# Performance work log

Measured on AMD Instinct MI355X. Metric: run time of the kernel, lower is better.

## Reference

```python
import jax, jax.numpy as jnp
import numpy as np

NA, NB, C = 50000, 50000, 128
E = 800000
S, IN, H, NBASES = 8, 64, 64, 8
NUM_LAYERS = 2
EPS = 1e-5


def setup_inputs() -> dict:
    key = jax.random.key(0)
    ks = jax.random.split(key, 16)
    inp = {
        'x_a': jax.random.normal(ks[0], (NA, C), jnp.float32),
        'x_b': jax.random.normal(ks[1], (NB, C), jnp.float32),
        'schema_x': jax.random.normal(ks[2], (S, IN), jnp.float32),
        'edge_ab': jax.random.randint(ks[3], (2, E), 0, NA, jnp.int32),
        'edge_ba': jax.random.randint(ks[4], (2, E), 0, NA, jnp.int32),
        'edge_aa': jax.random.randint(ks[5], (2, E), 0, NA, jnp.int32),
        'schema_edge_index': jax.random.randint(ks[6], (2, 24), 0, S, jnp.int32),
        'pre_W': jax.random.normal(ks[7], (H, IN), jnp.float32) * (1.0 / np.sqrt(IN)),
        'pre_b': jnp.zeros((H,), jnp.float32),
        'gcn_W': jax.random.normal(ks[8], (H, H), jnp.float32) * (1.0 / np.sqrt(H)),
        'gcn_b': jnp.zeros((H,), jnp.float32),
        'coeff_W': jax.random.normal(ks[9], (NBASES, 2 * H), jnp.float32) * (1.0 / np.sqrt(2 * H)),
        'coeff_b': jnp.zeros((NBASES,), jnp.float32),
        'bases': jax.random.normal(ks[10], (NUM_LAYERS, NBASES, C, C), jnp.float32) * (1.0 / np.sqrt(C)),
        'sage_bias': jnp.zeros((NUM_LAYERS, 3, C), jnp.float32),
        'ln_w': jnp.ones((NUM_LAYERS, 2, C), jnp.float32),
        'ln_b': jnp.zeros((NUM_LAYERS, 2, C), jnp.float32),
    }
    return inp


def _gcn_conv(x, ei, W, b):
    # PyG GCNConv: add self-loops, symmetric normalization, then linear.
    n = x.shape[0]
    loop = jnp.arange(n, dtype=ei.dtype)
    src = jnp.concatenate([ei[0], loop])
    dst = jnp.concatenate([ei[1], loop])
    deg = jax.ops.segment_sum(jnp.ones_like(dst, jnp.float32), dst, num_segments=n)
    dinv = jax.lax.rsqrt(jnp.maximum(deg, 1e-12))
    norm = dinv[src] * dinv[dst]  # [E+n]
    xw = x @ W.T  # [n, H]
    out = jax.ops.segment_sum(xw[src] * norm[:, None], dst, num_segments=n)
    return out + b


def _sage_conv(x_src, x_dst, ei, W, b):
    # PyG SAGEConv, aggr='mean': lin_l(mean_j x_src[j]) + lin_r(x_dst); lin_l.weight == lin_r.weight == W.
    n_dst = x_dst.shape[0]
    msg_sum = jax.ops.segment_sum(x_src[ei[0]], ei[1], num_segments=n_dst)
    cnt = jax.ops.segment_sum(jnp.ones(ei.shape[1], x_src.dtype), ei[1], num_segments=n_dst)
    mean = msg_sum / jnp.maximum(cnt, 1.0)[:, None]
    return (mean + x_dst) @ W.T + b


def _layer_norm(x, w, b):
    mu = jnp.mean(x, axis=-1, keepdims=True)
    var = jnp.mean(jnp.square(x - mu), axis=-1, keepdims=True)
    return (x - mu) * jax.lax.rsqrt(var + EPS) * w + b


def _edge_weight(sf_src, sf_dst, coeff_W, coeff_b, bases_l):
    combined = jnp.concatenate([sf_src, sf_dst], axis=0)  # [2H]
    coeffs = combined @ coeff_W.T + coeff_b  # [NBASES]
    return jnp.einsum('i,ijk->jk', coeffs, bases_l)  # [C, C]


def reference(x_a, x_b, schema_x, edge_ab, edge_ba, edge_aa, schema_edge_index,
              pre_W, pre_b, gcn_W, gcn_b, coeff_W, coeff_b, bases,
              sage_bias, ln_w, ln_b):
    # Schema GCN over the tiny table-level graph. table_to_index: a->0, b->1.
    h = schema_x @ pre_W.T + pre_b
    ori = h
    sf = jax.nn.relu(_gcn_conv(h, schema_edge_index, gcn_W, gcn_b))  # [S, H]

    for l in range(NUM_LAYERS):
        bases_l = bases[l]
        W_ab = _edge_weight(sf[0], sf[1], coeff_W, coeff_b, bases_l)
        W_ba = _edge_weight(sf[1], sf[0], coeff_W, coeff_b, bases_l)
        W_aa = _edge_weight(sf[0], sf[0], coeff_W, coeff_b, bases_l)
        # HeteroConv(aggr='sum'): sum SAGE outputs per destination node type.
        out_b = _sage_conv(x_a, x_b, edge_ab, W_ab, sage_bias[l, 0])
        out_a = (_sage_conv(x_b, x_a, edge_ba, W_ba, sage_bias[l, 1])
                 + _sage_conv(x_a, x_a, edge_aa, W_aa, sage_bias[l, 2]))
        x_a = jax.nn.relu(_layer_norm(out_a, ln_w[l, 0], ln_b[l, 0]))
        x_b = jax.nn.relu(_layer_norm(out_b, ln_w[l, 1], ln_b[l, 1]))

    return x_a, x_b, sf, ori
```

## Files before the change

kernel.cpp:

```cpp
#include <hip/hip_runtime.h>

#define NA 50000
#define NB 50000
#define NN 50000
#define CDIM 128
#define EDGES 800000
#define SS 8
#define INDIM 64
#define HDIM 64
#define NBASES 8
#define NBUCK 98
#define BSH 9

typedef __attribute__((ext_vector_type(8))) short bf16x8;
typedef __attribute__((ext_vector_type(4))) float f32x4;


__device__ __forceinline__ unsigned short f2bf(float f) {
    unsigned u = __float_as_uint(f);
    return (unsigned short)((u + 0x7FFFu + ((u >> 16) & 1u)) >> 16);
}

__global__ __launch_bounds__(512) void schema_kernel(
    const float* __restrict__ schema_x, const int* __restrict__ sei,
    const float* __restrict__ preW, const float* __restrict__ preb,
    const float* __restrict__ gcnW, const float* __restrict__ gcnb,
    const float* __restrict__ coW, const float* __restrict__ cob,
    float* __restrict__ out_sf, float* __restrict__ out_ori,
    float* __restrict__ coeffs)
{
    __shared__ float h[SS][HDIM];
    __shared__ float xw[SS][HDIM];
    __shared__ float sf[SS][HDIM];
    __shared__ float deg[SS];
    __shared__ float nrm[32];
    __shared__ int es[32], ed[32];

    int t = threadIdx.x;
    int i = t >> 6, j = t & 63;

    float acc = preb[j];
    for (int k = 0; k < INDIM; k++) acc += schema_x[i * INDIM + k] * preW[j * INDIM + k];
    h[i][j] = acc;
    out_ori[i * HDIM + j] = acc;
    if (t < SS) deg[t] = 0.0f;
    __syncthreads();

    if (t < 32) {
        int s, d;
        if (t < 24) { s = sei[t]; d = sei[24 + t]; }
        else        { s = t - 24; d = t - 24; }
        es[t] = s; ed[t] = d;
        atomicAdd(&deg[d], 1.0f);
    }
    __syncthreads();
    if (t < 32) {
        nrm[t] = rsqrtf(fmaxf(deg[es[t]], 1e-12f)) * rsqrtf(fmaxf(deg[ed[t]], 1e-12f));
    }
    float a2 = 0.0f;
    for (int k = 0; k < HDIM; k++) a2 += h[i][k] * gcnW[j * HDIM + k];
    xw[i][j] = a2;
    __syncthreads();

    float o = gcnb[j];
    for (int e = 0; e < 32; e++) {
        if (ed[e] == i) o += xw[es[e]][j] * nrm[e];
    }
    float s = fmaxf(o, 0.0f);
    sf[i][j] = s;
    out_sf[i * HDIM + j] = s;
    __syncthreads();

    if (t < 24) {
        int ty = t >> 3, ii = t & 7;
        int srow = (ty == 1) ? 1 : 0;
        int drow = (ty == 0) ? 1 : 0;
        float a = cob[ii];
        for (int k = 0; k < HDIM; k++) a += sf[srow][k] * coW[ii * (2 * HDIM) + k];
        for (int k = 0; k < HDIM; k++) a += sf[drow][k] * coW[ii * (2 * HDIM) + HDIM + k];
        coeffs[ty * 8 + ii] = a;
    }
}

__global__ __launch_bounds__(256) void build_w_kernel(
    const float* __restrict__ bases, const float* __restrict__ coeffs,
    unsigned short* __restrict__ Wbf)
{
    int idx = blockIdx.x * blockDim.x + threadIdx.x;
    int lt = idx >> 14;
    int jk = idx & 16383;
    int l = lt / 3, ty = lt % 3;
    float acc = 0.0f;
#pragma unroll
    for (int i = 0; i < NBASES; i++)
        acc += coeffs[ty * 8 + i] * bases[((size_t)(l * NBASES + i) << 14) + jk];
    Wbf[idx] = f2bf(acc);
}

__global__ __launch_bounds__(256) void tobf16_kernel(
    const float* __restrict__ in, unsigned short* __restrict__ out, int n)
{
    int i = (blockIdx.x * 256 + threadIdx.x) * 4;
    if (i >= n) return;
    float4 f = *(const float4*)(in + i);
    ushort4 o;
    o.x = f2bf(f.x); o.y = f2bf(f.y); o.z = f2bf(f.z); o.w = f2bf(f.w);
    *(ushort4*)(out + i) = o;
}

__global__ __launch_bounds__(256) void zero_rows_kernel(
    unsigned short* a0, unsigned short* b0, unsigned short* a1, unsigned short* b1)
{
    int t = threadIdx.x;
    int tab = t >> 6, w = t & 63;
    unsigned short* p = (tab == 0) ? a0 : (tab == 1) ? b0 : (tab == 2) ? a1 : b1;
    ((unsigned*)(p + (size_t)NN * CDIM))[w] = 0u;
}


__global__ __launch_bounds__(256) void bucket_count_kernel(
    const int* __restrict__ ab, const int* __restrict__ ba,
    const int* __restrict__ aa, int* __restrict__ bcnt)
{
    __shared__ int h[NBUCK];
    int t = threadIdx.x;
    int ty = blockIdx.y;
    const int* ei = (ty == 0) ? ab : (ty == 1) ? ba : aa;
    if (t < NBUCK) h[t] = 0;
    __syncthreads();
    int cb = blockIdx.x * 4096;
    int en = min(cb + 4096, EDGES);
    for (int e = cb + t; e < en; e += 256)
        atomicAdd(&h[ei[EDGES + e] >> BSH], 1);
    __syncthreads();
    if (t < NBUCK) atomicAdd(&bcnt[ty * NBUCK + t], h[t]);
}

__global__ __launch_bounds__(32) void bucket_scan_kernel(
    const int* __restrict__ bcnt, int* __restrict__ boff, int* __restrict__ bcur)
{
    int t = threadIdx.x;
    if (t < 3) {
        int run = 0;
        for (int i = 0; i < NBUCK; i++) {
            int c = bcnt[t * NBUCK + i];
            boff[t * (NBUCK + 1) + i] = run;
            bcur[t * NBUCK + i] = run;
            run += c;
        }
        boff[t * (NBUCK + 1) + NBUCK] = run;
    }
}

__global__ __launch_bounds__(256) void bucket_partition_kernel(
    const int* __restrict__ ab, const int* __restrict__ ba,
    const int* __restrict__ aa, int* __restrict__ bcur,
    unsigned* __restrict__ buf)
{
    __shared__ int h[NBUCK];
    __shared__ int basearr[NBUCK];
    __shared__ int cur[NBUCK];
    int t = threadIdx.x;
    int ty = blockIdx.y;
    const int* ei = (ty == 0) ? ab : (ty == 1) ? ba : aa;
    if (t < NBUCK) h[t] = 0;
    __syncthreads();
    int cb = blockIdx.x * 4096;
    int en = min(cb + 4096, EDGES);
    for (int e = cb + t; e < en; e += 256)
        atomicAdd(&h[ei[EDGES + e] >> BSH], 1);
    __syncthreads();
    if (t < NBUCK) {
        basearr[t] = atomicAdd(&bcur[ty * NBUCK + t], h[t]);
        cur[t] = 0;
    }
    __syncthreads();
    for (int e = cb + t; e < en; e += 256) {
        int src = ei[e], dst = ei[EDGES + e];
        int b = dst >> BSH;
        int r = atomicAdd(&cur[b], 1);
        buf[(size_t)ty * EDGES + basearr[b] + r] =
            ((unsigned)(dst & 511) << 16) | (unsigned)src;
    }
}

__global__ __launch_bounds__(256) void bucket_scatter_kernel(
    const unsigned* __restrict__ buf, const int* __restrict__ boff,
    int* __restrict__ rowptr, int* __restrict__ col)
{
    __shared__ int cnt[512];
    __shared__ int part[256];
    int t = threadIdx.x;
    int b = blockIdx.x, ty = blockIdx.y;
    int nstart = boff[ty * (NBUCK + 1) + b];
    int nend   = boff[ty * (NBUCK + 1) + b + 1];
    int n = nend - nstart;
    cnt[t] = 0; cnt[t + 256] = 0;
    __syncthreads();
    const unsigned* bb = buf + (size_t)ty * EDGES + nstart;
    for (int i = t; i < n; i += 256)
        atomicAdd(&cnt[bb[i] >> 16], 1);
    __syncthreads();
    int a0 = cnt[2 * t], a1 = cnt[2 * t + 1];
    int s = a0 + a1;
    part[t] = s;
    __syncthreads();
    for (int off = 1; off < 256; off <<= 1) {
        int v = (t >= off) ? part[t - off] : 0;
        __syncthreads();
        part[t] += v;
        __syncthreads();
    }
    int excl = part[t] - s;
    int p0 = excl, p1 = excl + a0;
    cnt[2 * t] = p0; cnt[2 * t + 1] = p1;
    int row0 = (b << BSH) + 2 * t;
    int rbase = ty * (NN + 1);
    if (row0 < NN)     rowptr[rbase + row0] = nstart + p0;
    if (row0 + 1 < NN) rowptr[rbase + row0 + 1] = nstart + p1;
    if (b == NBUCK - 1 && t == 255) rowptr[rbase + NN] = EDGES;
    __syncthreads();
    int* cc = col + (size_t)ty * EDGES + nstart;
    for (int i = t; i < n; i += 256) {
        unsigned pk = bb[i];
        int r = atomicAdd(&cnt[pk >> 16], 1);
        cc[r] = (int)(pk & 0xFFFFu);
    }
}


__device__ __forceinline__ float4 gather2_bf(
    const unsigned short* __restrict__ xsrc, const int* __restrict__ col,
    int s, int e, int half, int off)
{
    float4 g = {0.f, 0.f, 0.f, 0.f};
    int n = e - s;
    if (n > 0) {
        int cs[16];
#pragma unroll
        for (int j = 0; j < 16; j++) {
            int slot = s + 2 * j + half;
            int cc = col[min(slot, e - 1)];
            cs[j] = (slot < e) ? cc : NN;
        }
        uint2 v[16];
#pragma unroll
        for (int j = 0; j < 8; j++)
            v[j] = *(const uint2*)(xsrc + (size_t)cs[j] * CDIM + off);
        if (n > 16) {
#pragma unroll
            for (int j = 8; j < 16; j++)
                v[j] = *(const uint2*)(xsrc + (size_t)cs[j] * CDIM + off);
        } else {
#pragma unroll
            for (int j = 8; j < 16; j++) v[j] = make_uint2(0u, 0u);
        }
#pragma unroll
        for (int j = 0; j < 16; j++) {
            g.x += __uint_as_float(v[j].x << 16);
            g.y += __uint_as_float(v[j].x & 0xffff0000u);
            g.z += __uint_as_float(v[j].y << 16);
            g.w += __uint_as_float(v[j].y & 0xffff0000u);
        }
        for (int b2 = s + 32; b2 < e; b2 += 16) {
#pragma unroll
            for (int j = 0; j < 8; j++) {
                int slot = b2 + 2 * j + half;
                int cc = col[min(slot, e - 1)];
                int id = (slot < e) ? cc : NN;
                uint2 vv = *(const uint2*)(xsrc + (size_t)id * CDIM + off);
                g.x += __uint_as_float(vv.x << 16);
                g.y += __uint_as_float(vv.x & 0xffff0000u);
                g.z += __uint_as_float(vv.y << 16);
                g.w += __uint_as_float(vv.y & 0xffff0000u);
            }
        }
    }
    g.x += __shfl_xor(g.x, 32, 64);
    g.y += __shfl_xor(g.y, 32, 64);
    g.z += __shfl_xor(g.z, 32, 64);
    g.w += __shfl_xor(g.w, 32, 64);
    return g;
}

#define RROWS 32
#define USTR 136
#define SSTR 129

__global__ __launch_bounds__(256) void fuse_b_kernel(
    const unsigned short* __restrict__ xsrc, const float* __restrict__ xdst,
    const int* __restrict__ rowptr, const int* __restrict__ col,
    const unsigned short* __restrict__ Wbf, const float* __restrict__ bias,
    const float* __restrict__ lnw, const float* __restrict__ lnb,
    float* __restrict__ xnext, unsigned short* __restrict__ xnext_bf)
{
    __shared__ unsigned short Ubf[RROWS * USTR];
    __shared__ float stage[RROWS * SSTR];
    int t = threadIdx.x;
    int base = blockIdx.x * RROWS;
    int wv = t >> 6;
    int lane = t & 63;
    int half = lane >> 5, cl = lane & 31;
    int off = cl << 2;

    for (int rr = 0; rr < RROWS / 4; rr++) {
        int r = rr * 4 + wv;
        int row = base + r;
        if (row < NN) {
            int s = rowptr[row], e = rowptr[row + 1];
            float4 g = gather2_bf(xsrc, col, s, e, half, off);
            if (half == 0) {
                float inv = 1.0f / (float)max(e - s, 1);
                const float4 xv = *(const float4*)(xdst + (size_t)row * CDIM + off);
                ushort4 o;
                o.x = f2bf(g.x * inv + xv.x);
                o.y = f2bf(g.y * inv + xv.y);
                o.z = f2bf(g.z * inv + xv.z);
                o.w = f2bf(g.w * inv + xv.w);
                *(ushort4*)&Ubf[r * USTR + off] = o;
            }
        } else if (half == 0) {
            *(ushort4*)&Ubf[r * USTR + off] = make_ushort4(0, 0, 0, 0);
        }
    }
    __syncthreads();

    int qd = lane >> 4;
    int ln16 = lane & 15;
    f32x4 acc00 = {0.f,0.f,0.f,0.f}, acc01 = acc00, acc10 = acc00, acc11 = acc00;
#pragma unroll
    for (int ks = 0; ks < 4; ks++) {
        int koff = ks * 32 + qd * 8;
        bf16x8 a0 = *(const bf16x8*)&Ubf[(ln16) * USTR + koff];
        bf16x8 a1 = *(const bf16x8*)&Ubf[(16 + ln16) * USTR + koff];
        bf16x8 b0 = *(const bf16x8*)&Wbf[(size_t)((2 * wv + 0) * 16 + ln16) * CDIM + koff];
        bf16x8 b1 = *(const bf16x8*)&Wbf[(size_t)((2 * wv + 1) * 16 + ln16) * CDIM + koff];
        acc00 = __builtin_amdgcn_mfma_f32_16x16x32_bf16(a0, b0, acc00, 0, 0, 0);
        acc01 = __builtin_amdgcn_mfma_f32_16x16x32_bf16(a0, b1, acc01, 0, 0, 0);
        acc10 = __builtin_amdgcn_mfma_f32_16x16x32_bf16(a1, b0, acc10, 0, 0, 0);
        acc11 = __builtin_amdgcn_mfma_f32_16x16x32_bf16(a1, b1, acc11, 0, 0, 0);
    }
    {
        int c0 = (2 * wv + 0) * 16 + ln16;
        int c1 = (2 * wv + 1) * 16 + ln16;
#pragma unroll
        for (int i = 0; i < 4; i++) {
            int r0 = qd * 4 + i;
            stage[r0 * SSTR + c0] = acc00[i];
            stage[r0 * SSTR + c1] = acc01[i];
            stage[(16 + r0) * SSTR + c0] = acc10[i];
            stage[(16 + r0) * SSTR + c1] = acc11[i];
        }
    }
    __syncthreads();

    float b0v = bias[lane], b1v = bias[lane + 64];
    float lw0 = lnw[lane], lw1 = lnw[lane + 64];
    float lb0 = lnb[lane], lb1 = lnb[lane + 64];
    for (int rr = 0; rr < RROWS / 4; rr++) {
        int r = rr * 4 + wv;
        int row = base + r;
        if (row >= NN) continue;
        float v0 = stage[r * SSTR + lane] + b0v;
        float v1 = stage[r * SSTR + lane + 64] + b1v;
        float s = v0 + v1, s2 = v0 * v0 + v1 * v1;
#pragma unroll
        for (int o2 = 32; o2 > 0; o2 >>= 1) {
            s  += __shfl_xor(s,  o2, 64);
            s2 += __shfl_xor(s2, o2, 64);
        }
        float mu = s * (1.0f / CDIM);
        float var = s2 * (1.0f / CDIM) - mu * mu;
        float rs = rsqrtf(var + 1e-5f);
        float o0 = fmaxf((v0 - mu) * rs * lw0 + lb0, 0.0f);
        float o1 = fmaxf((v1 - mu) * rs * lw1 + lb1, 0.0f);
        size_t oi = (size_t)row * CDIM;
        xnext[oi + lane] = o0;
        xnext[oi + lane + 64] = o1;
        if (xnext_bf) {
            xnext_bf[oi + lane] = f2bf(o0);
            xnext_bf[oi + lane + 64] = f2bf(o1);
        }
    }
}

__global__ __launch_bounds__(256) void fuse_a_kernel(
    const unsigned short* __restrict__ xsrc1, const int* __restrict__ rowptr1, const int* __restrict__ col1,
    const unsigned short* __restrict__ xsrc2, const int* __restrict__ rowptr2, const int* __restrict__ col2,
    const float* __restrict__ xdst,
    const unsigned short* __restrict__ W1bf, const unsigned short* __restrict__ W2bf,
    const float* __restrict__ bias1, const float* __restrict__ bias2,
    const float* __restrict__ lnw, const float* __restrict__ lnb,
    float* __restrict__ xnext, unsigned short* __restrict__ xnext_bf)
{
    __shared__ unsigned short Ubf[RROWS * USTR];
    __shared__ unsigned short Vbf[RROWS * USTR];
    __shared__ float stage[RROWS * SSTR];
    int t = threadIdx.x;
    int base = blockIdx.x * RROWS;
    int wv = t >> 6;
    int lane = t & 63;
    int half = lane >> 5, cl = lane & 31;
    int off = cl << 2;

    for (int rr = 0; rr < RROWS / 4; rr++) {
        int r = rr * 4 + wv;
        int row = base + r;
        if (row < NN) {
            int s1 = rowptr1[row], e1 = rowptr1[row + 1];
            float4 g1 = gather2_bf(xsrc1, col1, s1, e1, half, off);
            int s2 = rowptr2[row], e2 = rowptr2[row + 1];
            float4 g2 = gather2_bf(xsrc2, col2, s2, e2, half, off);
            if (half == 0) {
                const float4 xv = *(const float4*)(xdst + (size_t)row * CDIM + off);
                float i1 = 1.0f / (float)max(e1 - s1, 1);
                float i2 = 1.0f / (float)max(e2 - s2, 1);
                ushort4 ou, ov;
                ou.x = f2bf(g1.x * i1 + xv.x); ou.y = f2bf(g1.y * i1 + xv.y);
                ou.z = f2bf(g1.z * i1 + xv.z); ou.w = f2bf(g1.w * i1 + xv.w);
                ov.x = f2bf(g2.x * i2 + xv.x); ov.y = f2bf(g2.y * i2 + xv.y);
                ov.z = f2bf(g2.z * i2 + xv.z); ov.w = f2bf(g2.w * i2 + xv.w);
                *(ushort4*)&Ubf[r * USTR + off] = ou;
                *(ushort4*)&Vbf[r * USTR + off] = ov;
            }
        } else if (half == 0) {
            *(ushort4*)&Ubf[r * USTR + off] = make_ushort4(0, 0, 0, 0);
            *(ushort4*)&Vbf[r * USTR + off] = make_ushort4(0, 0, 0, 0);
        }
    }
    __syncthreads();

    int qd = lane >> 4;
    int ln16 = lane & 15;
    f32x4 acc00 = {0.f,0.f,0.f,0.f}, acc01 = acc00, acc10 = acc00, acc11 = acc00;
#pragma unroll
    for (int ks = 0; ks < 4; ks++) {
        int koff = ks * 32 + qd * 8;
        bf16x8 aU0 = *(const bf16x8*)&Ubf[(ln16) * USTR + koff];
        bf16x8 aU1 = *(const bf16x8*)&Ubf[(16 + ln16) * USTR + koff];
        bf16x8 aV0 = *(const bf16x8*)&Vbf[(ln16) * USTR + koff];
        bf16x8 aV1 = *(const bf16x8*)&Vbf[(16 + ln16) * USTR + koff];
        size_t wrow0 = (size_t)((2 * wv + 0) * 16 + ln16) * CDIM + koff;
        size_t wrow1 = (size_t)((2 * wv + 1) * 16 + ln16) * CDIM + koff;
        bf16x8 b10 = *(const bf16x8*)&W1bf[wrow0];
        bf16x8 b11 = *(const bf16x8*)&W1bf[wrow1];
        bf16x8 b20 = *(const bf16x8*)&W2bf[wrow0];
        bf16x8 b21 = *(const bf16x8*)&W2bf[wrow1];
        acc00 = __builtin_amdgcn_mfma_f32_16x16x32_bf16(aU0, b10, acc00, 0, 0, 0);
        acc01 = __builtin_amdgcn_mfma_f32_16x16x32_bf16(aU0, b11, acc01, 0, 0, 0);
        acc10 = __builtin_amdgcn_mfma_f32_16x16x32_bf16(aU1, b10, acc10, 0, 0, 0);
        acc11 = __builtin_amdgcn_mfma_f32_16x16x32_bf16(aU1, b11, acc11, 0, 0, 0);
        acc00 = __builtin_amdgcn_mfma_f32_16x16x32_bf16(aV0, b20, acc00, 0, 0, 0);
        acc01 = __builtin_amdgcn_mfma_f32_16x16x32_bf16(aV0, b21, acc01, 0, 0, 0);
        acc10 = __builtin_amdgcn_mfma_f32_16x16x32_bf16(aV1, b20, acc10, 0, 0, 0);
        acc11 = __builtin_amdgcn_mfma_f32_16x16x32_bf16(aV1, b21, acc11, 0, 0, 0);
    }
    {
        int c0 = (2 * wv + 0) * 16 + ln16;
        int c1 = (2 * wv + 1) * 16 + ln16;
#pragma unroll
        for (int i = 0; i < 4; i++) {
            int r0 = qd * 4 + i;
            stage[r0 * SSTR + c0] = acc00[i];
            stage[r0 * SSTR + c1] = acc01[i];
            stage[(16 + r0) * SSTR + c0] = acc10[i];
            stage[(16 + r0) * SSTR + c1] = acc11[i];
        }
    }
    __syncthreads();

    float b0v = bias1[lane] + bias2[lane];
    float b1v = bias1[lane + 64] + bias2[lane + 64];
    float lw0 = lnw[lane], lw1 = lnw[lane + 64];
    float lb0 = lnb[lane], lb1 = lnb[lane + 64];
    for (int rr = 0; rr < RROWS / 4; rr++) {
        int r = rr * 4 + wv;
        int row = base + r;
        if (row >= NN) continue;
        float v0 = stage[r * SSTR + lane] + b0v;
        float v1 = stage[r * SSTR + lane + 64] + b1v;
        float s = v0 + v1, s2 = v0 * v0 + v1 * v1;
#pragma unroll
        for (int o2 = 32; o2 > 0; o2 >>= 1) {
            s  += __shfl_xor(s,  o2, 64);
            s2 += __shfl_xor(s2, o2, 64);
        }
        float mu = s * (1.0f / CDIM);
        float var = s2 * (1.0f / CDIM) - mu * mu;
        float rs = rsqrtf(var + 1e-5f);
        float o0 = fmaxf((v0 - mu) * rs * lw0 + lb0, 0.0f);
        float o1 = fmaxf((v1 - mu) * rs * lw1 + lb1, 0.0f);
        size_t oi = (size_t)row * CDIM;
        xnext[oi + lane] = o0;
        xnext[oi + lane + 64] = o1;
        if (xnext_bf) {
            xnext_bf[oi + lane] = f2bf(o0);
            xnext_bf[oi + lane + 64] = f2bf(o1);
        }
    }
}

extern "C" void kernel_launch(void* const* d_in, const int* in_sizes, int n_in,
                              void* d_out, int out_size, void* d_ws, size_t ws_size,
                              hipStream_t stream)
{
    const float* x_a      = (const float*)d_in[0];
    const float* x_b      = (const float*)d_in[1];
    const float* schema_x = (const float*)d_in[2];
    const int*   e_ab     = (const int*)d_in[3];
    const int*   e_ba     = (const int*)d_in[4];
    const int*   e_aa     = (const int*)d_in[5];
    const int*   sei      = (const int*)d_in[6];
    const float* preW     = (const float*)d_in[7];
    const float* preb     = (const float*)d_in[8];
    const float* gcnW     = (const float*)d_in[9];
    const float* gcnb     = (const float*)d_in[10];
    const float* coW      = (const float*)d_in[11];
    const float* cob      = (const float*)d_in[12];
    const float* bases    = (const float*)d_in[13];
    const float* sbias    = (const float*)d_in[14];
    const float* lnw      = (const float*)d_in[15];
    const float* lnb      = (const float*)d_in[16];

    float* out     = (float*)d_out;
    float* out_xa  = out;
    float* out_xb  = out + 6400000;
    float* out_sf  = out + 12800000;
    float* out_ori = out + 12800512;

    float* ws = (float*)d_ws;
    int*      col    = (int*)ws;
    int*      rowptr = (int*)(ws + 2400000);
    unsigned* buf    = (unsigned*)(ws + 2550016);
    int*      bcnt   = (int*)(ws + 4950016);
    int*      boff   = (int*)(ws + 4950320);
    int*      bcur   = (int*)(ws + 4950624);
    float* xa_buf = ws + 4950928;
    float* xb_buf = ws + 11350928;
    unsigned short* Wbf = (unsigned short*)(ws + 17750928);
    float* coeffs = ws + 17800080;
    unsigned short* xa_bf0 = (unsigned short*)(ws + 17800112);
    unsigned short* xb_bf0 = (unsigned short*)(ws + 21000176);
    unsigned short* xa_bf1 = (unsigned short*)(ws + 24200240);
    unsigned short* xb_bf1 = (unsigned short*)(ws + 27400304);

    schema_kernel<<<1, 512, 0, stream>>>(schema_x, sei, preW, preb, gcnW, gcnb,
                                         coW, cob, out_sf, out_ori, coeffs);
    build_w_kernel<<<384, 256, 0, stream>>>(bases, coeffs, Wbf);

    tobf16_kernel<<<(NA * CDIM / 4 + 255) / 256, 256, 0, stream>>>(x_a, xa_bf0, NA * CDIM);
    tobf16_kernel<<<(NB * CDIM / 4 + 255) / 256, 256, 0, stream>>>(x_b, xb_bf0, NB * CDIM);
    zero_rows_kernel<<<1, 256, 0, stream>>>(xa_bf0, xb_bf0, xa_bf1, xb_bf1);

    hipMemsetAsync(bcnt, 0, 3 * NBUCK * sizeof(int), stream);
    dim3 cgrid((EDGES + 4095) / 4096, 3);
    bucket_count_kernel<<<cgrid, 256, 0, stream>>>(e_ab, e_ba, e_aa, bcnt);
    bucket_scan_kernel<<<1, 32, 0, stream>>>(bcnt, boff, bcur);
    bucket_partition_kernel<<<cgrid, 256, 0, stream>>>(e_ab, e_ba, e_aa, bcur, buf);
    dim3 sgrid(NBUCK, 3);
    bucket_scatter_kernel<<<sgrid, 256, 0, stream>>>(buf, boff, rowptr, col);

    const int* rp_ab = rowptr;
    const int* rp_ba = rowptr + (NN + 1);
    const int* rp_aa = rowptr + 2 * (NN + 1);
    const int* col_ab = col;
    const int* col_ba = col + EDGES;
    const int* col_aa = col + 2 * EDGES;

    const int fgrid = (NN + RROWS - 1) / RROWS;

    for (int l = 0; l < 2; l++) {
        const float* xa_cur = (l == 0) ? x_a : xa_buf;
        const float* xb_cur = (l == 0) ? x_b : xb_buf;
        const unsigned short* xa_bf = (l == 0) ? xa_bf0 : xa_bf1;
        const unsigned short* xb_bf = (l == 0) ? xb_bf0 : xb_bf1;
        const unsigned short* Wab = Wbf + (size_t)(l * 3 + 0) * 16384;
        const unsigned short* Wba = Wbf + (size_t)(l * 3 + 1) * 16384;
        const unsigned short* Waa = Wbf + (size_t)(l * 3 + 2) * 16384;
        float* xa_nxt = (l == 0) ? xa_buf : out_xa;
        float* xb_nxt = (l == 0) ? xb_buf : out_xb;
        unsigned short* xa_nbf = (l == 0) ? xa_bf1 : nullptr;
        unsigned short* xb_nbf = (l == 0) ? xb_bf1 : nullptr;

        fuse_b_kernel<<<fgrid, 256, 0, stream>>>(
            xa_bf, xb_cur, rp_ab, col_ab, Wab,
            sbias + (size_t)(l * 3 + 0) * 128,
            lnw + (size_t)(l * 2 + 1) * 128, lnb + (size_t)(l * 2 + 1) * 128,
            xb_nxt, xb_nbf);
        fuse_a_kernel<<<fgrid, 256, 0, stream>>>(
            xb_bf, rp_ba, col_ba, xa_bf, rp_aa, col_aa, xa_cur,
            Wba, Waa,
            sbias + (size_t)(l * 3 + 1) * 128, sbias + (size_t)(l * 3 + 2) * 128,
            lnw + (size_t)(l * 2 + 0) * 128, lnb + (size_t)(l * 2 + 0) * 128,
            xa_nxt, xa_nbf);
    }
}
```

Measured before the change: 556.7 us.

## Alias shared staging buffers, raise occupancy bound, and specialise short-row gather

The bf16 input tiles and the fp32 output staging buffer now share one shared-memory region, with an added barrier between the MFMA reads and the staging writes. This cuts per-block LDS so more blocks fit per CU. Launch bounds now request 8 waves-per-EU occupancy. The gather gets a separate path for rows with at most 16 neighbours that issues only 8 loads, avoiding the wasted padded second half. The risks are register spilling under the tighter launch bound and the cost of the extra barrier.

```diff
diff --git a/kernel.cpp b/kernel.cpp
--- a/kernel.cpp
+++ b/kernel.cpp
@@ -236,43 +236,56 @@
     float4 g = {0.f, 0.f, 0.f, 0.f};
     int n = e - s;
     if (n > 0) {
-        int cs[16];
-#pragma unroll
-        for (int j = 0; j < 16; j++) {
-            int slot = s + 2 * j + half;
-            int cc = col[min(slot, e - 1)];
-            cs[j] = (slot < e) ? cc : NN;
-        }
-        uint2 v[16];
-#pragma unroll
-        for (int j = 0; j < 8; j++)
-            v[j] = *(const uint2*)(xsrc + (size_t)cs[j] * CDIM + off);
-        if (n > 16) {
-#pragma unroll
-            for (int j = 8; j < 16; j++)
+        if (n <= 16) {
+            int cs[8];
+#pragma unroll
+            for (int j = 0; j < 8; j++) {
+                int slot = s + 2 * j + half;
+                int cc = col[min(slot, e - 1)];
+                cs[j] = (slot < e) ? cc : NN;
+            }
+            uint2 v[8];
+#pragma unroll
+            for (int j = 0; j < 8; j++)
                 v[j] = *(const uint2*)(xsrc + (size_t)cs[j] * CDIM + off);
+#pragma unroll
+            for (int j = 0; j < 8; j++) {
+                g.x += __uint_as_float(v[j].x << 16);
+                g.y += __uint_as_float(v[j].x & 0xffff0000u);
+                g.z += __uint_as_float(v[j].y << 16);
+                g.w += __uint_as_float(v[j].y & 0xffff0000u);
+            }
         } else {
-#pragma unroll
-            for (int j = 8; j < 16; j++) v[j] = make_uint2(0u, 0u);
-        }
-#pragma unroll
-        for (int j = 0; j < 16; j++) {
-            g.x += __uint_as_float(v[j].x << 16);
-            g.y += __uint_as_float(v[j].x & 0xffff0000u);
-            g.z += __uint_as_float(v[j].y << 16);
-            g.w += __uint_as_float(v[j].y & 0xffff0000u);
-        }
-        for (int b2 = s + 32; b2 < e; b2 += 16) {
-#pragma unroll
-            for (int j = 0; j < 8; j++) {
-                int slot = b2 + 2 * j + half;
+            int cs[16];
+#pragma unroll
+            for (int j = 0; j < 16; j++) {
+                int slot = s + 2 * j + half;
                 int cc = col[min(slot, e - 1)];
-                int id = (slot < e) ? cc : NN;
-                uint2 vv = *(const uint2*)(xsrc + (size_t)id * CDIM + off);
-                g.x += __uint_as_float(vv.x << 16);
-                g.y += __uint_as_float(vv.x & 0xffff0000u);
-                g.z += __uint_as_float(vv.y << 16);
-                g.w += __uint_as_float(vv.y & 0xffff0000u);
+                cs[j] = (slot < e) ? cc : NN;
+            }
+            uint2 v[16];
+#pragma unroll
+            for (int j = 0; j < 16; j++)
+                v[j] = *(const uint2*)(xsrc + (size_t)cs[j] * CDIM + off);
+#pragma unroll
+            for (int j = 0; j < 16; j++) {
+                g.x += __uint_as_float(v[j].x << 16);
+                g.y += __uint_as_float(v[j].x & 0xffff0000u);
+                g.z += __uint_as_float(v[j].y << 16);
+                g.w += __uint_as_float(v[j].y & 0xffff0000u);
+            }
+            for (int b2 = s + 32; b2 < e; b2 += 16) {
+#pragma unroll
+                for (int j = 0; j < 8; j++) {
+                    int slot = b2 + 2 * j + half;
+                    int cc = col[min(slot, e - 1)];
+                    int id = (slot < e) ? cc : NN;
+                    uint2 vv = *(const uint2*)(xsrc + (size_t)id * CDIM + off);
+                    g.x += __uint_as_float(vv.x << 16);
+                    g.y += __uint_as_float(vv.x & 0xffff0000u);
+                    g.z += __uint_as_float(vv.y << 16);
+                    g.w += __uint_as_float(vv.y & 0xffff0000u);
+                }
             }
         }
     }
@@ -287,15 +300,16 @@
 #define USTR 136
 #define SSTR 129
 
-__global__ __launch_bounds__(256) void fuse_b_kernel(
+__global__ __launch_bounds__(256, 8) void fuse_b_kernel(
     const unsigned short* __restrict__ xsrc, const float* __restrict__ xdst,
     const int* __restrict__ rowptr, const int* __restrict__ col,
     const unsigned short* __restrict__ Wbf, const float* __restrict__ bias,
     const float* __restrict__ lnw, const float* __restrict__ lnb,
     float* __restrict__ xnext, unsigned short* __restrict__ xnext_bf)
 {
-    __shared__ unsigned short Ubf[RROWS * USTR];
-    __shared__ float stage[RROWS * SSTR];
+    __shared__ float4 smraw[1032];
+    unsigned short* Ubf = (unsigned short*)smraw;
+    float* stage = (float*)smraw;
     int t = threadIdx.x;
     int base = blockIdx.x * RROWS;
     int wv = t >> 6;
@@ -340,6 +354,7 @@
         acc10 = __builtin_amdgcn_mfma_f32_16x16x32_bf16(a1, b0, acc10, 0, 0, 0);
         acc11 = __builtin_amdgcn_mfma_f32_16x16x32_bf16(a1, b1, acc11, 0, 0, 0);
     }
+    __syncthreads();
     {
         int c0 = (2 * wv + 0) * 16 + ln16;
         int c1 = (2 * wv + 1) * 16 + ln16;
@@ -384,7 +399,7 @@
     }
 }
 
-__global__ __launch_bounds__(256) void fuse_a_kernel(
+__global__ __launch_bounds__(256, 8) void fuse_a_kernel(
     const unsigned short* __restrict__ xsrc1, const int* __restrict__ rowptr1, const int* __restrict__ col1,
     const unsigned short* __restrict__ xsrc2, const int* __restrict__ rowptr2, const int* __restrict__ col2,
     const float* __restrict__ xdst,
@@ -393,9 +408,10 @@
     const float* __restrict__ lnw, const float* __restrict__ lnb,
     float* __restrict__ xnext, unsigned short* __restrict__ xnext_bf)
 {
-    __shared__ unsigned short Ubf[RROWS * USTR];
-    __shared__ unsigned short Vbf[RROWS * USTR];
-    __shared__ float stage[RROWS * SSTR];
+    __shared__ float4 smraw[1088];
+    unsigned short* Ubf = (unsigned short*)smraw;
+    unsigned short* Vbf = Ubf + RROWS * USTR;
+    float* stage = (float*)smraw;
     int t = threadIdx.x;
     int base = blockIdx.x * RROWS;
     int wv = t >> 6;
@@ -455,6 +471,7 @@
         acc10 = __builtin_amdgcn_mfma_f32_16x16x32_bf16(aV1, b20, acc10, 0, 0, 0);
         acc11 = __builtin_amdgcn_mfma_f32_16x16x32_bf16(aV1, b21, acc11, 0, 0, 0);
     }
+    __syncthreads();
     {
         int c0 = (2 * wv + 0) * 16 + ln16;
         int c1 = (2 * wv + 1) * 16 + ln16;
```

Result: no change. 549.4 us (-1.3%).
